# Optimization experiments

Hardware: AMD Instinct MI355X
Metric: run time of the kernel (lower is better)

Reference implementation:

```python
import jax, jax.numpy as jnp
import numpy as np

EMBED_DIM = 1024
N_HEADS = 16
HEAD_DIM = EMBED_DIM // N_HEADS


def setup_inputs() -> dict:
    key = jax.random.key(0)
    ks = jax.random.split(key, 5)
    B, T, C = 4, 2048, EMBED_DIM
    s = 0.02
    return {
        "x": jax.random.normal(ks[0], (B, T, C), dtype=jnp.float32),
        "w_qkv": jax.random.normal(ks[1], (C, 3 * C), dtype=jnp.float32) * s,
        "b_qkv": jnp.zeros((3 * C,), dtype=jnp.float32),
        "w_proj": jax.random.normal(ks[2], (C, C), dtype=jnp.float32) * s,
        "b_proj": jnp.zeros((C,), dtype=jnp.float32),
    }


def reference(x, w_qkv, b_qkv, w_proj, b_proj):
    B, T, C = x.shape
    H, D = N_HEADS, HEAD_DIM
    qkv = x @ w_qkv + b_qkv  # [B,T,3C]
    q, k, v = jnp.split(qkv, 3, axis=-1)
    # [B,H,T,D]
    q = q.reshape(B, T, H, D).transpose(0, 2, 1, 3)
    k = k.reshape(B, T, H, D).transpose(0, 2, 1, 3)
    v = v.reshape(B, T, H, D).transpose(0, 2, 1, 3)
    scale = jnp.asarray(D, x.dtype) ** -0.5
    att = jnp.einsum("bhqd,bhkd->bhqk", q, k) * scale  # [B,H,T,T]
    causal = jnp.tril(jnp.ones((T, T), dtype=bool))
    att = jnp.where(causal, att, jnp.asarray(-jnp.inf, att.dtype))
    att = jax.nn.softmax(att, axis=-1)
    out = jnp.einsum("bhqk,bhkd->bhqd", att, v)  # [B,H,T,D]
    out = out.transpose(0, 2, 1, 3).reshape(B, T, C)
    return out @ w_proj + b_proj
```

## Files before the change

kernel.cpp:

```cpp
#include <hip/hip_runtime.h>
#include <hip/hip_bf16.h>


typedef __bf16 bf16x8 __attribute__((ext_vector_type(8)));
typedef float f32x4 __attribute__((ext_vector_type(4)));
typedef unsigned short u16x8 __attribute__((ext_vector_type(8)));
typedef unsigned short u16x4 __attribute__((ext_vector_type(4)));
typedef unsigned int u32;

#define LOG2E 1.44269504088896340736f
#define NEG_INF (-__builtin_inff())

#define AS_GLOBAL(p) ((const __attribute__((address_space(1))) u32*)(p))
#define AS_LDS(p) ((__attribute__((address_space(3))) u32*)(p))

__device__ __forceinline__ unsigned short f2bf(float f) {
  unsigned int u = __builtin_bit_cast(unsigned int, f);
  u += 0x7fff + ((u >> 16) & 1);
  return (unsigned short)(u >> 16);
}

__device__ __forceinline__ u32 cvt_pk_bf16(float lo, float hi) {
  u32 r;
  asm("v_cvt_pk_bf16_f32 %0, %1, %2" : "=v"(r) : "v"(lo), "v"(hi));
  return r;
}

__device__ __forceinline__ bf16x8 ld_frag(const unsigned short* p) {
  return __builtin_bit_cast(bf16x8, *reinterpret_cast<const u16x8*>(p));
}

__global__ void k_convert(const float* __restrict__ in, unsigned short* __restrict__ out, int n4) {
  int i = blockIdx.x * blockDim.x + threadIdx.x;
  int stride = gridDim.x * blockDim.x;
  for (; i < n4; i += stride) {
    float4 v = reinterpret_cast<const float4*>(in)[i];
    u16x4 o = { f2bf(v.x), f2bf(v.y), f2bf(v.z), f2bf(v.w) };
    reinterpret_cast<u16x4*>(out)[i] = o;
  }
}

__global__ void k_transpose(const float* __restrict__ in, unsigned short* __restrict__ out,
                            int K, int N, int scaleN, float scl) {
  __shared__ float tile[32][33];
  int n0 = blockIdx.x * 32, k0 = blockIdx.y * 32;
  int tx = threadIdx.x & 31, ty = threadIdx.x >> 5;
#pragma unroll
  for (int i = 0; i < 4; i++)
    tile[ty + i * 8][tx] = in[(size_t)(k0 + ty + i * 8) * N + n0 + tx];
  __syncthreads();
#pragma unroll
  for (int i = 0; i < 4; i++) {
    int n = n0 + ty + i * 8;
    float v = tile[tx][ty + i * 8];
    if (n < scaleN) v *= scl;
    out[(size_t)n * K + k0 + tx] = f2bf(v);
  }
}

__global__ void k_scale_bias(const float* __restrict__ in, float* __restrict__ out,
                             int n, int scaleN, float scl) {
  int i = blockIdx.x * blockDim.x + threadIdx.x;
  if (i < n) out[i] = (i < scaleN) ? in[i] * scl : in[i];
}

template <bool BF16_OUT>
__global__ __launch_bounds__(256) void k_gemm(
    const unsigned short* __restrict__ A, const unsigned short* __restrict__ Bt,
    const float* __restrict__ bias, void* __restrict__ Cv, int M, int N, int K) {
  constexpr int BK = 64;
  __shared__ unsigned short Asm[128][BK];
  __shared__ unsigned short Bsm[128][BK];
  const int tid = threadIdx.x;
  const int lane = tid & 63, w = tid >> 6;
  const int wr = w >> 1, wc = w & 1;

  int bid = blockIdx.y * gridDim.x + blockIdx.x;
  int cpx = (gridDim.x * gridDim.y) >> 3;
  int swz = (bid & 7) * cpx + (bid >> 3);
  const int brow = (swz % gridDim.x) * 128, bcol = (swz / gridDim.x) * 128;

  const int r0 = lane & 15, kq = lane >> 4;

  f32x4 acc[4][4] = {};

  const int srow = lane >> 3, scol = (lane & 7) * 8;

  for (int k0 = 0; k0 < K; k0 += BK) {
    __syncthreads();
#pragma unroll
    for (int q = 0; q < 4; q++) {
      int c = w * 4 + q;
      const unsigned short* ga = &A[(size_t)(brow + c * 8 + srow) * K + k0 + scol];
      const unsigned short* gb = &Bt[(size_t)(bcol + c * 8 + srow) * K + k0 + scol];
      __builtin_amdgcn_global_load_lds(AS_GLOBAL(ga), AS_LDS(&Asm[c * 8][0]), 16, 0, 0);
      __builtin_amdgcn_global_load_lds(AS_GLOBAL(gb), AS_LDS(&Bsm[c * 8][0]), 16, 0, 0);
    }
    __syncthreads();
#pragma unroll
    for (int c = 0; c < 2; c++) {
      bf16x8 af[4], bfr[4];
#pragma unroll
      for (int m = 0; m < 4; m++)
        af[m] = ld_frag(&Asm[wr * 64 + m * 16 + r0][c * 32 + kq * 8]);
#pragma unroll
      for (int n = 0; n < 4; n++)
        bfr[n] = ld_frag(&Bsm[wc * 64 + n * 16 + r0][c * 32 + kq * 8]);
      __builtin_amdgcn_s_setprio(1);
#pragma unroll
      for (int m = 0; m < 4; m++)
#pragma unroll
        for (int n = 0; n < 4; n++)
          acc[m][n] = __builtin_amdgcn_mfma_f32_16x16x32_bf16(af[m], bfr[n], acc[m][n], 0, 0, 0);
      __builtin_amdgcn_s_setprio(0);
    }
  }

  const int orow = kq * 4;
#pragma unroll
  for (int n = 0; n < 4; n++) {
#pragma unroll
    for (int m = 0; m < 4; m++) {
      int col = bcol + wc * 64 + n * 16 + r0;
      float bv = bias[col];
#pragma unroll
      for (int r = 0; r < 4; r++) {
        int row = brow + wr * 64 + m * 16 + orow + r;
        float v = acc[m][n][r] + bv;
        if (BF16_OUT)
          ((unsigned short*)Cv)[(size_t)row * N + col] = f2bf(v);
        else
          ((float*)Cv)[(size_t)row * N + col] = v;
      }
    }
  }
}

__global__ __launch_bounds__(256) void k_flash(const unsigned short* __restrict__ qkv,
                                               unsigned short* __restrict__ att, int T) {
  constexpr int C3 = 3072, C = 1024;
  __shared__ unsigned short Ksm[2][64][72];
  __shared__ unsigned short Vsm[2][64][72];

  const int tid = threadIdx.x, lane = tid & 63, w = tid >> 6;
  const int bh = blockIdx.x;
  const int qt = gridDim.y - 1 - blockIdx.y;
  const int b = bh >> 4, h = bh & 15;
  const int q0 = qt * 64;
  const int r0 = lane & 15, kq = lane >> 4;

  const size_t rowbase = (size_t)b * T * C3;

  bf16x8 qf[2];
  {
    const unsigned short* qp = &qkv[rowbase + (size_t)(q0 + w * 16 + r0) * C3 + h * 64];
    qf[0] = ld_frag(&qp[kq * 8]);
    qf[1] = ld_frag(&qp[32 + kq * 8]);
  }

  f32x4 accO[4] = {};
  f32x4 ls4 = {0.f, 0.f, 0.f, 0.f};
  float m_run = NEG_INF;
  const int q_my = q0 + w * 16 + r0;

  const int stk = tid >> 3, sd8 = (tid & 7) * 8;
  const unsigned short* kbase = &qkv[rowbase + (size_t)stk * C3 + h * 64 + sd8 + C];
  constexpr size_t PSTRIDE = (size_t)32 * C3;

  u16x8 kreg[2], vreg[2];
  auto LOADT = [&](size_t off) {
#pragma unroll
    for (int p = 0; p < 2; p++) {
      kreg[p] = *reinterpret_cast<const u16x8*>(kbase + off + p * PSTRIDE);
      vreg[p] = *reinterpret_cast<const u16x8*>(kbase + off + p * PSTRIDE + C);
    }
  };
  auto WRITET = [&](int buf) {
#pragma unroll
    for (int p = 0; p < 2; p++) {
      int tkk = p * 32 + stk;
      *reinterpret_cast<u16x8*>(&Ksm[buf][tkk][sd8]) = kreg[p];
      int tkx = tkk ^ sd8;
#pragma unroll
      for (int i = 0; i < 8; i++) Vsm[buf][sd8 + i][tkx] = vreg[p][i];
    }
  };

  auto TILE = [&](int buf, int k0, bool diag) {
    const unsigned short(*Ks)[72] = Ksm[buf];
    const unsigned short(*Vs)[72] = Vsm[buf];

    f32x4 st[4];
    __builtin_amdgcn_s_setprio(1);
#pragma unroll
    for (int s = 0; s < 4; s++) {
      f32x4 a = {};
      a = __builtin_amdgcn_mfma_f32_16x16x32_bf16(ld_frag(&Ks[s * 16 + r0][kq * 8]), qf[0], a, 0, 0, 0);
      a = __builtin_amdgcn_mfma_f32_16x16x32_bf16(ld_frag(&Ks[s * 16 + r0][32 + kq * 8]), qf[1], a, 0, 0, 0);
      st[s] = a;
    }
    __builtin_amdgcn_s_setprio(0);

    f32x4 sv4[4];
    if (diag) {
#pragma unroll
      for (int s = 0; s < 4; s++)
#pragma unroll
        for (int r = 0; r < 4; r++) {
          int kg = k0 + s * 16 + kq * 4 + r;
          sv4[s][r] = (kg > q_my) ? NEG_INF : st[s][r];
        }
    } else {
#pragma unroll
      for (int s = 0; s < 4; s++) sv4[s] = st[s];
    }

    f32x4 m4 = __builtin_elementwise_max(__builtin_elementwise_max(sv4[0], sv4[1]),
                                         __builtin_elementwise_max(sv4[2], sv4[3]));
    float mx = fmaxf(fmaxf(m4[0], m4[1]), fmaxf(m4[2], m4[3]));

    if (__any(mx > m_run + 8.f)) {
      mx = fmaxf(mx, __shfl_xor(mx, 16));
      mx = fmaxf(mx, __shfl_xor(mx, 32));
      float mn = fmaxf(m_run, mx);
      float corr = exp2f(m_run - mn);
      m_run = mn;
      ls4 *= corr;
      float cq[4];
#pragma unroll
      for (int r = 0; r < 4; r++) cq[r] = __shfl(corr, kq * 4 + r);
#pragma unroll
      for (int n = 0; n < 4; n++)
#pragma unroll
        for (int r = 0; r < 4; r++) accO[n][r] *= cq[r];
    }

    f32x4 pv4[4];
#pragma unroll
    for (int s = 0; s < 4; s++) {
      f32x4 d = sv4[s] - m_run;
      f32x4 p = { exp2f(d[0]), exp2f(d[1]), exp2f(d[2]), exp2f(d[3]) };
      pv4[s] = p;
      ls4 += p;
    }

    __builtin_amdgcn_s_setprio(1);
#pragma unroll
    for (int t = 0; t < 2; t++) {
      u32 pd[4];
      pd[0] = cvt_pk_bf16(pv4[2 * t][0], pv4[2 * t][1]);
      pd[1] = cvt_pk_bf16(pv4[2 * t][2], pv4[2 * t][3]);
      pd[2] = cvt_pk_bf16(pv4[2 * t + 1][0], pv4[2 * t + 1][1]);
      pd[3] = cvt_pk_bf16(pv4[2 * t + 1][2], pv4[2 * t + 1][3]);
      bf16x8 pa = __builtin_bit_cast(bf16x8, *reinterpret_cast<u16x8*>(pd));
#pragma unroll
      for (int n = 0; n < 4; n++) {
        int d = n * 16 + r0;
        int swzb = d & 56;
        const u16x4 lo = *reinterpret_cast<const u16x4*>(&Vs[d][(t * 32 + kq * 4) ^ swzb]);
        const u16x4 hi = *reinterpret_cast<const u16x4*>(&Vs[d][(t * 32 + 16 + kq * 4) ^ swzb]);
        u16x8 vb;
#pragma unroll
        for (int i = 0; i < 4; i++) { vb[i] = lo[i]; vb[4 + i] = hi[i]; }
        accO[n] = __builtin_amdgcn_mfma_f32_16x16x32_bf16(
            pa, __builtin_bit_cast(bf16x8, vb), accO[n], 0, 0, 0);
      }
    }
    __builtin_amdgcn_s_setprio(0);
  };

  int buf = 0;
  LOADT(0);
  WRITET(0);
  size_t koff = (size_t)64 * C3;
  for (int kt = 0; kt < qt; kt++) {
    __syncthreads();
    LOADT(koff);
    koff += (size_t)64 * C3;
    TILE(buf, kt * 64, false);
    WRITET(buf ^ 1);
    buf ^= 1;
  }
  __syncthreads();
  TILE(buf, qt * 64, true);

  float l_run = ls4[0] + ls4[1] + ls4[2] + ls4[3];
  l_run += __shfl_xor(l_run, 16);
  l_run += __shfl_xor(l_run, 32);
  float lr[4];
#pragma unroll
  for (int r = 0; r < 4; r++) lr[r] = 1.f / __shfl(l_run, kq * 4 + r);
#pragma unroll
  for (int n = 0; n < 4; n++) {
#pragma unroll
    for (int r = 0; r < 4; r++) {
      int qrow = q0 + w * 16 + kq * 4 + r;
      float v = accO[n][r] * lr[r];
      att[((size_t)b * T + qrow) * C + h * 64 + n * 16 + r0] = f2bf(v);
    }
  }
}

extern "C" void kernel_launch(void* const* d_in, const int* in_sizes, int n_in,
                              void* d_out, int out_size, void* d_ws, size_t ws_size,
                              hipStream_t stream) {
  const float* x = (const float*)d_in[0];
  const float* w_qkv = (const float*)d_in[1];
  const float* b_qkv = (const float*)d_in[2];
  const float* w_proj = (const float*)d_in[3];
  const float* b_proj = (const float*)d_in[4];

  constexpr int B = 4, T = 2048, C = 1024, C3 = 3072;
  constexpr int M = B * T;
  constexpr float SCL = 0.125f * LOG2E;

  unsigned short* x_bf = (unsigned short*)d_ws;
  unsigned short* wqkvT = x_bf + (size_t)M * C;
  unsigned short* wprojT = wqkvT + (size_t)C3 * C;
  unsigned short* qkv = wprojT + (size_t)C * C;
  unsigned short* att = qkv + (size_t)M * C3;
  float* bias_s = (float*)(att + (size_t)M * C);

  hipLaunchKernelGGL(k_convert, dim3(2048), dim3(256), 0, stream, x, x_bf, M * C / 4);
  hipLaunchKernelGGL(k_transpose, dim3(C3 / 32, C / 32), dim3(256), 0, stream,
                     w_qkv, wqkvT, C, C3, C, SCL);
  hipLaunchKernelGGL(k_transpose, dim3(C / 32, C / 32), dim3(256), 0, stream,
                     w_proj, wprojT, C, C, 0, 1.f);
  hipLaunchKernelGGL(k_scale_bias, dim3((C3 + 255) / 256), dim3(256), 0, stream,
                     b_qkv, bias_s, C3, C, SCL);
  hipLaunchKernelGGL((k_gemm<true>), dim3(M / 128, C3 / 128), dim3(256), 0, stream,
                     x_bf, wqkvT, bias_s, (void*)qkv, M, C3, C);
  hipLaunchKernelGGL(k_flash, dim3(64, 32), dim3(256), 0, stream, qkv, att, T);
  hipLaunchKernelGGL((k_gemm<false>), dim3(M / 128, C / 128), dim3(256), 0, stream,
                     att, wprojT, b_proj, d_out, M, C, C);
}
```

Before: 193.8 us.

## Process two 16-row query blocks per wave in flash attention, drop GEMM tile swizzle

Each flash-attention wave now handles 32 query rows (two 16-row sub-blocks), so one workgroup covers 128 queries and every K/V fragment read from LDS feeds twice as many MFMAs. The grid is halved, and a per-sub-block causal check skips tiles and masking where not needed. Launch bounds ask for 3 blocks per CU to limit register growth. Separately, the GEMM drops its block-index swizzle for plain row/column mapping, which may hurt L2 reuse. The risks are higher register pressure, fewer workgroups, and more imbalance from the causal split.

```diff
diff --git a/kernel.cpp b/kernel.cpp
--- a/kernel.cpp
+++ b/kernel.cpp
@@ -74,12 +74,7 @@
   const int tid = threadIdx.x;
   const int lane = tid & 63, w = tid >> 6;
   const int wr = w >> 1, wc = w & 1;
-
-  int bid = blockIdx.y * gridDim.x + blockIdx.x;
-  int cpx = (gridDim.x * gridDim.y) >> 3;
-  int swz = (bid & 7) * cpx + (bid >> 3);
-  const int brow = (swz % gridDim.x) * 128, bcol = (swz / gridDim.x) * 128;
-
+  const int brow = blockIdx.x * 128, bcol = blockIdx.y * 128;
   const int r0 = lane & 15, kq = lane >> 4;
 
   f32x4 acc[4][4] = {};
@@ -136,32 +131,35 @@
   }
 }
 
-__global__ __launch_bounds__(256) void k_flash(const unsigned short* __restrict__ qkv,
-                                               unsigned short* __restrict__ att, int T) {
+__global__ __launch_bounds__(256, 3) void k_flash(const unsigned short* __restrict__ qkv,
+                                                  unsigned short* __restrict__ att, int T) {
   constexpr int C3 = 3072, C = 1024;
   __shared__ unsigned short Ksm[2][64][72];
   __shared__ unsigned short Vsm[2][64][72];
 
   const int tid = threadIdx.x, lane = tid & 63, w = tid >> 6;
   const int bh = blockIdx.x;
-  const int qt = gridDim.y - 1 - blockIdx.y;
+  const int qtp = gridDim.y - 1 - blockIdx.y;
   const int b = bh >> 4, h = bh & 15;
-  const int q0 = qt * 64;
+  const int q0 = qtp * 128;
   const int r0 = lane & 15, kq = lane >> 4;
 
   const size_t rowbase = (size_t)b * T * C3;
-
-  bf16x8 qf[2];
+  const int qb0 = q0 + w * 32, qb1 = qb0 + 16;
+
+  bf16x8 qf[2][2];
   {
-    const unsigned short* qp = &qkv[rowbase + (size_t)(q0 + w * 16 + r0) * C3 + h * 64];
-    qf[0] = ld_frag(&qp[kq * 8]);
-    qf[1] = ld_frag(&qp[32 + kq * 8]);
-  }
-
-  f32x4 accO[4] = {};
-  f32x4 ls4 = {0.f, 0.f, 0.f, 0.f};
-  float m_run = NEG_INF;
-  const int q_my = q0 + w * 16 + r0;
+    const unsigned short* qp0 = &qkv[rowbase + (size_t)(qb0 + r0) * C3 + h * 64];
+    qf[0][0] = ld_frag(&qp0[kq * 8]);
+    qf[0][1] = ld_frag(&qp0[32 + kq * 8]);
+    const unsigned short* qp1 = qp0 + (size_t)16 * C3;
+    qf[1][0] = ld_frag(&qp1[kq * 8]);
+    qf[1][1] = ld_frag(&qp1[32 + kq * 8]);
+  }
+
+  f32x4 accO[2][4] = {};
+  f32x4 ls4[2] = {{0.f,0.f,0.f,0.f},{0.f,0.f,0.f,0.f}};
+  float m_run[2] = {NEG_INF, NEG_INF};
 
   const int stk = tid >> 3, sd8 = (tid & 7) * 8;
   const unsigned short* kbase = &qkv[rowbase + (size_t)stk * C3 + h * 64 + sd8 + C];
@@ -186,84 +184,100 @@
     }
   };
 
-  auto TILE = [&](int buf, int k0, bool diag) {
+  auto TILE = [&](int buf, int k0) {
+    if (k0 > qb1 + 15) return;
     const unsigned short(*Ks)[72] = Ksm[buf];
     const unsigned short(*Vs)[72] = Vsm[buf];
 
-    f32x4 st[4];
+    f32x4 st[2][4];
     __builtin_amdgcn_s_setprio(1);
 #pragma unroll
     for (int s = 0; s < 4; s++) {
-      f32x4 a = {};
-      a = __builtin_amdgcn_mfma_f32_16x16x32_bf16(ld_frag(&Ks[s * 16 + r0][kq * 8]), qf[0], a, 0, 0, 0);
-      a = __builtin_amdgcn_mfma_f32_16x16x32_bf16(ld_frag(&Ks[s * 16 + r0][32 + kq * 8]), qf[1], a, 0, 0, 0);
-      st[s] = a;
+      bf16x8 kf0 = ld_frag(&Ks[s * 16 + r0][kq * 8]);
+      bf16x8 kf1 = ld_frag(&Ks[s * 16 + r0][32 + kq * 8]);
+#pragma unroll
+      for (int u = 0; u < 2; u++) {
+        f32x4 a = {};
+        a = __builtin_amdgcn_mfma_f32_16x16x32_bf16(kf0, qf[u][0], a, 0, 0, 0);
+        a = __builtin_amdgcn_mfma_f32_16x16x32_bf16(kf1, qf[u][1], a, 0, 0, 0);
+        st[u][s] = a;
+      }
     }
     __builtin_amdgcn_s_setprio(0);
 
-    f32x4 sv4[4];
-    if (diag) {
-#pragma unroll
-      for (int s = 0; s < 4; s++)
-#pragma unroll
-        for (int r = 0; r < 4; r++) {
-          int kg = k0 + s * 16 + kq * 4 + r;
-          sv4[s][r] = (kg > q_my) ? NEG_INF : st[s][r];
-        }
-    } else {
-#pragma unroll
-      for (int s = 0; s < 4; s++) sv4[s] = st[s];
-    }
-
-    f32x4 m4 = __builtin_elementwise_max(__builtin_elementwise_max(sv4[0], sv4[1]),
-                                         __builtin_elementwise_max(sv4[2], sv4[3]));
-    float mx = fmaxf(fmaxf(m4[0], m4[1]), fmaxf(m4[2], m4[3]));
-
-    if (__any(mx > m_run + 8.f)) {
-      mx = fmaxf(mx, __shfl_xor(mx, 16));
-      mx = fmaxf(mx, __shfl_xor(mx, 32));
-      float mn = fmaxf(m_run, mx);
-      float corr = exp2f(m_run - mn);
-      m_run = mn;
-      ls4 *= corr;
-      float cq[4];
-#pragma unroll
-      for (int r = 0; r < 4; r++) cq[r] = __shfl(corr, kq * 4 + r);
-#pragma unroll
-      for (int n = 0; n < 4; n++)
-#pragma unroll
-        for (int r = 0; r < 4; r++) accO[n][r] *= cq[r];
-    }
-
-    f32x4 pv4[4];
-#pragma unroll
-    for (int s = 0; s < 4; s++) {
-      f32x4 d = sv4[s] - m_run;
-      f32x4 p = { exp2f(d[0]), exp2f(d[1]), exp2f(d[2]), exp2f(d[3]) };
-      pv4[s] = p;
-      ls4 += p;
+    u32 pd[2][2][4];
+#pragma unroll
+    for (int u = 0; u < 2; u++) {
+      const int qbu = u ? qb1 : qb0;
+      const int qmy = qbu + r0;
+      f32x4 sv[4];
+      if (k0 + 63 > qbu) {
+#pragma unroll
+        for (int s = 0; s < 4; s++)
+#pragma unroll
+          for (int r = 0; r < 4; r++) {
+            int kg = k0 + s * 16 + kq * 4 + r;
+            sv[s][r] = (kg > qmy) ? NEG_INF : st[u][s][r];
+          }
+      } else {
+#pragma unroll
+        for (int s = 0; s < 4; s++) sv[s] = st[u][s];
+      }
+
+      f32x4 m4 = __builtin_elementwise_max(__builtin_elementwise_max(sv[0], sv[1]),
+                                           __builtin_elementwise_max(sv[2], sv[3]));
+      float mx = fmaxf(fmaxf(m4[0], m4[1]), fmaxf(m4[2], m4[3]));
+
+      if (__any(mx > m_run[u] + 8.f)) {
+        mx = fmaxf(mx, __shfl_xor(mx, 16));
+        mx = fmaxf(mx, __shfl_xor(mx, 32));
+        float mn = fmaxf(m_run[u], mx);
+        float corr = exp2f(m_run[u] - mn);
+        m_run[u] = mn;
+        ls4[u] *= corr;
+        float cq[4];
+#pragma unroll
+        for (int r = 0; r < 4; r++) cq[r] = __shfl(corr, kq * 4 + r);
+#pragma unroll
+        for (int n = 0; n < 4; n++)
+#pragma unroll
+          for (int r = 0; r < 4; r++) accO[u][n][r] *= cq[r];
+      }
+
+#pragma unroll
+      for (int s = 0; s < 4; s++) {
+        f32x4 d = sv[s] - m_run[u];
+        f32x4 p = { exp2f(d[0]), exp2f(d[1]), exp2f(d[2]), exp2f(d[3]) };
+        sv[s] = p;
+        ls4[u] += p;
+      }
+      pd[u][0][0] = cvt_pk_bf16(sv[0][0], sv[0][1]);
+      pd[u][0][1] = cvt_pk_bf16(sv[0][2], sv[0][3]);
+      pd[u][0][2] = cvt_pk_bf16(sv[1][0], sv[1][1]);
+      pd[u][0][3] = cvt_pk_bf16(sv[1][2], sv[1][3]);
+      pd[u][1][0] = cvt_pk_bf16(sv[2][0], sv[2][1]);
+      pd[u][1][1] = cvt_pk_bf16(sv[2][2], sv[2][3]);
+      pd[u][1][2] = cvt_pk_bf16(sv[3][0], sv[3][1]);
+      pd[u][1][3] = cvt_pk_bf16(sv[3][2], sv[3][3]);
     }
 
     __builtin_amdgcn_s_setprio(1);
 #pragma unroll
     for (int t = 0; t < 2; t++) {
-      u32 pd[4];
-      pd[0] = cvt_pk_bf16(pv4[2 * t][0], pv4[2 * t][1]);
-      pd[1] = cvt_pk_bf16(pv4[2 * t][2], pv4[2 * t][3]);
-      pd[2] = cvt_pk_bf16(pv4[2 * t + 1][0], pv4[2 * t + 1][1]);
-      pd[3] = cvt_pk_bf16(pv4[2 * t + 1][2], pv4[2 * t + 1][3]);
-      bf16x8 pa = __builtin_bit_cast(bf16x8, *reinterpret_cast<u16x8*>(pd));
+      bf16x8 pa0 = __builtin_bit_cast(bf16x8, *reinterpret_cast<u16x8*>(pd[0][t]));
+      bf16x8 pa1 = __builtin_bit_cast(bf16x8, *reinterpret_cast<u16x8*>(pd[1][t]));
 #pragma unroll
       for (int n = 0; n < 4; n++) {
         int d = n * 16 + r0;
         int swzb = d & 56;
         const u16x4 lo = *reinterpret_cast<const u16x4*>(&Vs[d][(t * 32 + kq * 4) ^ swzb]);
         const u16x4 hi = *reinterpret_cast<const u16x4*>(&Vs[d][(t * 32 + 16 + kq * 4) ^ swzb]);
-        u16x8 vb;
-#pragma unroll
-        for (int i = 0; i < 4; i++) { vb[i] = lo[i]; vb[4 + i] = hi[i]; }
-        accO[n] = __builtin_amdgcn_mfma_f32_16x16x32_bf16(
-            pa, __builtin_bit_cast(bf16x8, vb), accO[n], 0, 0, 0);
+        u16x8 vbw;
+#pragma unroll
+        for (int i = 0; i < 4; i++) { vbw[i] = lo[i]; vbw[4 + i] = hi[i]; }
+        bf16x8 vb = __builtin_bit_cast(bf16x8, vbw);
+        accO[0][n] = __builtin_amdgcn_mfma_f32_16x16x32_bf16(pa0, vb, accO[0][n], 0, 0, 0);
+        accO[1][n] = __builtin_amdgcn_mfma_f32_16x16x32_bf16(pa1, vb, accO[1][n], 0, 0, 0);
       }
     }
     __builtin_amdgcn_s_setprio(0);
@@ -273,30 +287,35 @@
   LOADT(0);
   WRITET(0);
   size_t koff = (size_t)64 * C3;
-  for (int kt = 0; kt < qt; kt++) {
+  const int nkt = (q0 + 128) >> 6;
+  for (int kt = 0; kt < nkt - 1; kt++) {
     __syncthreads();
     LOADT(koff);
     koff += (size_t)64 * C3;
-    TILE(buf, kt * 64, false);
+    TILE(buf, kt * 64);
     WRITET(buf ^ 1);
     buf ^= 1;
   }
   __syncthreads();
-  TILE(buf, qt * 64, true);
-
-  float l_run = ls4[0] + ls4[1] + ls4[2] + ls4[3];
-  l_run += __shfl_xor(l_run, 16);
-  l_run += __shfl_xor(l_run, 32);
-  float lr[4];
-#pragma unroll
-  for (int r = 0; r < 4; r++) lr[r] = 1.f / __shfl(l_run, kq * 4 + r);
-#pragma unroll
-  for (int n = 0; n < 4; n++) {
-#pragma unroll
-    for (int r = 0; r < 4; r++) {
-      int qrow = q0 + w * 16 + kq * 4 + r;
-      float v = accO[n][r] * lr[r];
-      att[((size_t)b * T + qrow) * C + h * 64 + n * 16 + r0] = f2bf(v);
+  TILE(buf, (nkt - 1) * 64);
+
+#pragma unroll
+  for (int u = 0; u < 2; u++) {
+    const int qbu = u ? qb1 : qb0;
+    float l = ls4[u][0] + ls4[u][1] + ls4[u][2] + ls4[u][3];
+    l += __shfl_xor(l, 16);
+    l += __shfl_xor(l, 32);
+    float lr[4];
+#pragma unroll
+    for (int r = 0; r < 4; r++) lr[r] = 1.f / __shfl(l, kq * 4 + r);
+#pragma unroll
+    for (int n = 0; n < 4; n++) {
+#pragma unroll
+      for (int r = 0; r < 4; r++) {
+        int qrow = qbu + kq * 4 + r;
+        float v = accO[u][n][r] * lr[r];
+        att[((size_t)b * T + qrow) * C + h * 64 + n * 16 + r0] = f2bf(v);
+      }
     }
   }
 }
@@ -330,7 +349,7 @@
                      b_qkv, bias_s, C3, C, SCL);
   hipLaunchKernelGGL((k_gemm<true>), dim3(M / 128, C3 / 128), dim3(256), 0, stream,
                      x_bf, wqkvT, bias_s, (void*)qkv, M, C3, C);
-  hipLaunchKernelGGL(k_flash, dim3(64, 32), dim3(256), 0, stream, qkv, att, T);
+  hipLaunchKernelGGL(k_flash, dim3(64, 16), dim3(256), 0, stream, qkv, att, T);
   hipLaunchKernelGGL((k_gemm<false>), dim3(M / 128, C / 128), dim3(256), 0, stream,
                      att, wprojT, b_proj, d_out, M, C, C);
 }
```

Result: faster. 180.4 us (-6.9%).
